# Kernel optimization log

Measured on AMD Instinct MI355X. Metric: run time of the kernel, lower is better.

## Reference

```python
import jax, jax.numpy as jnp
import numpy as np

N, E, F, FE, H, R = 100000, 3200000, 2, 7, 64, 500
BN_EPS = 1e-5
LEAKY_SLOPE = 0.01


def _bn(h, g, b):
    # BatchNorm1d in training mode: batch statistics over the node axis
    m = h.mean(0)
    v = h.var(0)
    return (h - m) * jax.lax.rsqrt(v + BN_EPS) * g + b


def _gine_conv(x, src, dst, edge_attr, eps, el_w, el_b, w1, b1, g, bt, w2, b2):
    # message: relu(x_j + Lin(edge_attr)); aggregate: scatter-add at dst
    msg = jax.nn.relu(x[src] + edge_attr @ el_w + el_b)          # [E, d]
    agg = jax.ops.segment_sum(msg, dst, num_segments=N)          # [N, d]
    h = (1.0 + eps) * x + agg
    # nn: Linear -> BN -> ReLU -> Linear -> ReLU
    h = jax.nn.relu(_bn(h @ w1 + b1, g, bt))
    return jax.nn.relu(h @ w2 + b2)


def setup_inputs() -> dict:
    key = jax.random.key(0)
    ks = jax.random.split(key, 16)
    r = lambda k, s, sc=0.1: jax.random.normal(k, s, dtype=jnp.float32) * sc
    return {
        "x": jax.random.normal(ks[0], (N, F), dtype=jnp.float32),
        "edge_attr": jax.random.normal(ks[1], (E, FE), dtype=jnp.float32),
        "edge_index": jax.random.randint(ks[2], (2, E), 0, N),
        "epoch": 1,
        "eps1": jnp.zeros((), jnp.float32),
        "el1_w": r(ks[3], (FE, F)), "el1_b": jnp.zeros((F,), jnp.float32),
        "n1_w1": r(ks[4], (F, H)), "n1_b1": jnp.zeros((H,), jnp.float32),
        "n1_g": jnp.ones((H,), jnp.float32), "n1_bt": jnp.zeros((H,), jnp.float32),
        "n1_w2": r(ks[5], (H, H)), "n1_b2": jnp.zeros((H,), jnp.float32),
        "eps2": jnp.zeros((), jnp.float32),
        "el2_w": r(ks[6], (FE, H)), "el2_b": jnp.zeros((H,), jnp.float32),
        "n2_w1": r(ks[7], (H, H)), "n2_b1": jnp.zeros((H,), jnp.float32),
        "n2_g": jnp.ones((H,), jnp.float32), "n2_bt": jnp.zeros((H,), jnp.float32),
        "n2_w2": r(ks[8], (H, H)), "n2_b2": jnp.zeros((H,), jnp.float32),
        "reg_w": r(ks[9], (H, R)), "reg_b": jnp.zeros((R,), jnp.float32),
        "end_w": r(ks[10], (R, 1)), "end_b": jnp.zeros((1,), jnp.float32),
    }


def reference(x, edge_attr, edge_index, epoch,
              eps1, el1_w, el1_b, n1_w1, n1_b1, n1_g, n1_bt, n1_w2, n1_b2,
              eps2, el2_w, el2_b, n2_w1, n2_b1, n2_g, n2_bt, n2_w2, n2_b2,
              reg_w, reg_b, end_w, end_b):
    src, dst = edge_index[0], edge_index[1]
    out = _gine_conv(x, src, dst, edge_attr, eps1, el1_w, el1_b,
                     n1_w1, n1_b1, n1_g, n1_bt, n1_w2, n1_b2)
    for _ in range(3 - 1):  # num_layers=3, shared conv2 weights
        out = _gine_conv(out, src, dst, edge_attr, eps2, el2_w, el2_b,
                         n2_w1, n2_b1, n2_g, n2_bt, n2_w2, n2_b2)
    # dropout p=0.0 -> identity; epoch only resets dropout, no effect here
    out = out @ reg_w + reg_b
    out = jnp.where(out >= 0, out, LEAKY_SLOPE * out)  # LeakyReLU
    out = out @ end_w + end_b                            # [N, 1]
    return out
```

## Files before the change

### kernel.cpp

```cpp
#include <hip/hip_runtime.h>
#include <hip/hip_fp16.h>

#define NN 100000
#define NE 3200000
#define NB 196
#define NCH 256
#define CH 12500

__device__ inline unsigned pkh(float a, float b) {
  __half2 h;
  h.x = __float2half(a);
  h.y = __float2half(b);
  unsigned u;
  __builtin_memcpy(&u, &h, 4);
  return u;
}
__device__ inline float2 uph(unsigned u) {
  __half2 h;
  __builtin_memcpy(&h, &u, 4);
  return __half22float2(h);
}
__device__ inline float h1f(unsigned short v) {
  __half h;
  __builtin_memcpy(&h, &v, 2);
  return __half2float(h);
}
__device__ inline unsigned short f1h(float f) {
  __half h = __float2half(f);
  unsigned short u;
  __builtin_memcpy(&u, &h, 2);
  return u;
}

__global__ __launch_bounds__(256) void count_kernel(const int* __restrict__ dst,
                                                    int* __restrict__ cnt) {
  int stride = gridDim.x * 256;
  for (int e = blockIdx.x * 256 + threadIdx.x; e < NE; e += stride)
    atomicAdd(&cnt[dst[e]], 1);
}

__global__ __launch_bounds__(1024) void scan_kernel(const int* __restrict__ cnt,
                                                    int* __restrict__ rowptr,
                                                    int* __restrict__ ofs) {
  __shared__ int bsum[1024];
  int tid = threadIdx.x;
  const int CHS = (NN + 1023) / 1024;
  int lo = tid * CHS, hi = lo + CHS < NN ? lo + CHS : NN;
  if (lo > NN) lo = NN;
  if (hi < lo) hi = lo;
  int s = 0;
  for (int i = lo; i < hi; i++) s += cnt[i];
  bsum[tid] = s;
  __syncthreads();
  for (int off = 1; off < 1024; off <<= 1) {
    int v = bsum[tid];
    int u = (tid >= off) ? bsum[tid - off] : 0;
    __syncthreads();
    bsum[tid] = v + u;
    __syncthreads();
  }
  int pre = (tid == 0) ? 0 : bsum[tid - 1];
  for (int i = lo; i < hi; i++) {
    int cv = cnt[i];
    rowptr[i] = pre;
    ofs[i] = pre;
    pre += cv;
  }
  if (tid == 1023) rowptr[NN] = pre;
}

__global__ __launch_bounds__(256) void binit_kernel(const int* __restrict__ rowptr,
                                                    int* __restrict__ binofs) {
  int t = threadIdx.x;
  if (t < NB) binofs[t] = rowptr[t * 512];
}

__global__ __launch_bounds__(256) void localsort_kernel(
    const int* __restrict__ src, const int* __restrict__ dst,
    const float* __restrict__ ea, int* __restrict__ binofs,
    uint4* __restrict__ stageR, int* __restrict__ stageS) {
  __shared__ int hist[NB];
  __shared__ int base[NB];
  int tid = threadIdx.x;
  int c0 = blockIdx.x * CH;
  int c1 = c0 + CH;
  if (tid < NB) hist[tid] = 0;
  __syncthreads();
  for (int e = c0 + tid; e < c1; e += 256)
    atomicAdd(&hist[dst[e] >> 9], 1);
  __syncthreads();
  if (tid < NB) {
    base[tid] = atomicAdd(&binofs[tid], hist[tid]);
    hist[tid] = 0;
  }
  __syncthreads();
  for (int e = c0 + tid; e < c1; e += 256) {
    int dn = dst[e];
    int sn = src[e];
    int b = dn >> 9;
    float av[7];
#pragma unroll
    for (int k = 0; k < 7; k++) av[k] = ea[e * 7 + k];
    int lp = atomicAdd(&hist[b], 1);
    int pos = base[b] + lp;
    uint4 r;
    r.x = pkh(av[0], av[1]);
    r.y = pkh(av[2], av[3]);
    r.z = pkh(av[4], av[5]);
    r.w = (unsigned)f1h(av[6]) | (((unsigned)dn & 511u) << 16);
    stageR[pos] = r;
    stageS[pos] = sn;
  }
}

__global__ __launch_bounds__(256) void binsort2_kernel(
    const int* __restrict__ rowptr, const uint4* __restrict__ stageR,
    const int* __restrict__ stageS, int* __restrict__ ofs,
    uint4* __restrict__ erec, int* __restrict__ esrc,
    const float* __restrict__ x, const float* __restrict__ elw,
    const float* __restrict__ elb, float* __restrict__ agg1) {
  float w0[7], w1r[7];
#pragma unroll
  for (int k = 0; k < 7; k++) { w0[k] = elw[k * 2]; w1r[k] = elw[k * 2 + 1]; }
  float b0 = elb[0], b1 = elb[1];
  int bin = blockIdx.x >> 1, half = blockIdx.x & 1;
  int nlo = bin * 512;
  int nhi = nlo + 512 < NN ? nlo + 512 : NN;
  int r0 = rowptr[nlo], r1 = rowptr[nhi];
  int mid = (r0 + r1) >> 1;
  int lo = half ? mid : r0;
  int hi = half ? r1 : mid;
  for (int i = lo + threadIdx.x; i < hi; i += 256) {
    uint4 u = stageR[i];
    int sn = stageS[i];
    int dn = nlo + (int)(u.w >> 16);
    int pos = atomicAdd(&ofs[dn], 1);
    erec[pos] = u;
    esrc[pos] = sn;
    float2 q0 = uph(u.x), q1 = uph(u.y), q2 = uph(u.z);
    float e6 = h1f((unsigned short)(u.w & 0xFFFFu));
    float m0 = b0, m1 = b1;
    m0 = fmaf(q0.x, w0[0], m0); m1 = fmaf(q0.x, w1r[0], m1);
    m0 = fmaf(q0.y, w0[1], m0); m1 = fmaf(q0.y, w1r[1], m1);
    m0 = fmaf(q1.x, w0[2], m0); m1 = fmaf(q1.x, w1r[2], m1);
    m0 = fmaf(q1.y, w0[3], m0); m1 = fmaf(q1.y, w1r[3], m1);
    m0 = fmaf(q2.x, w0[4], m0); m1 = fmaf(q2.x, w1r[4], m1);
    m0 = fmaf(q2.y, w0[5], m0); m1 = fmaf(q2.y, w1r[5], m1);
    m0 = fmaf(e6, w0[6], m0);   m1 = fmaf(e6, w1r[6], m1);
    m0 = fmaxf(m0 + x[sn * 2 + 0], 0.f);
    m1 = fmaxf(m1 + x[sn * 2 + 1], 0.f);
    unsafeAtomicAdd(&agg1[dn * 2 + 0], m0);
    unsafeAtomicAdd(&agg1[dn * 2 + 1], m1);
  }
}

__global__ __launch_bounds__(256) void scatter1_kernel(
    const int* __restrict__ dst, int* __restrict__ ofs, int* __restrict__ eid_s) {
  int stride = gridDim.x * 256;
  for (int e = blockIdx.x * 256 + threadIdx.x; e < NE; e += stride) {
    int pos = atomicAdd(&ofs[dst[e]], 1);
    eid_s[pos] = e;
  }
}

__global__ __launch_bounds__(256) void l1agg_kernel(
    const int* __restrict__ rowptr, const int* __restrict__ eid_s,
    const int* __restrict__ src, const float* __restrict__ ea,
    const float* __restrict__ x, const float* __restrict__ elw,
    const float* __restrict__ elb, float* __restrict__ agg) {
  float w0[7], w1r[7];
#pragma unroll
  for (int k = 0; k < 7; k++) { w0[k] = elw[k * 2]; w1r[k] = elw[k * 2 + 1]; }
  float b0 = elb[0], b1 = elb[1];
  int stride = gridDim.x * 256;
  for (int n = blockIdx.x * 256 + threadIdx.x; n < NN; n += stride) {
    int r0 = rowptr[n], r1 = rowptr[n + 1];
    float a0 = 0.f, a1 = 0.f;
    for (int i = r0; i < r1; i++) {
      int e = eid_s[i];
      int sn = src[e];
      float m0 = b0, m1 = b1;
#pragma unroll
      for (int k = 0; k < 7; k++) {
        float a = ea[e * 7 + k];
        m0 = fmaf(a, w0[k], m0);
        m1 = fmaf(a, w1r[k], m1);
      }
      m0 = fmaxf(m0 + x[sn * 2 + 0], 0.f);
      m1 = fmaxf(m1 + x[sn * 2 + 1], 0.f);
      a0 += m0; a1 += m1;
    }
    agg[n * 2 + 0] = a0;
    agg[n * 2 + 1] = a1;
  }
}

#define PROJH(m, u) do { \
  float2 q0 = uph((u).x), q1 = uph((u).y), q2 = uph((u).z), q3 = uph((u).w); \
  m = bel; \
  m = fmaf(q0.x, wel[0], m); m = fmaf(q0.y, wel[1], m); \
  m = fmaf(q1.x, wel[2], m); m = fmaf(q1.y, wel[3], m); \
  m = fmaf(q2.x, wel[4], m); m = fmaf(q2.y, wel[5], m); \
  m = fmaf(q3.x, wel[6], m); } while (0)

__global__ __launch_bounds__(256) void gine64h_kernel(
    const int* __restrict__ rowptr, const uint4* __restrict__ erec,
    const int* __restrict__ esrc, const float* __restrict__ xin,
    const unsigned short* __restrict__ xh, const float* __restrict__ elw,
    const float* __restrict__ elb, const float* __restrict__ w1,
    const float* __restrict__ b1, const float* __restrict__ eps_p,
    float* __restrict__ tbuf, float* __restrict__ stats) {
  __shared__ float wl[64 * 64];
  __shared__ float hb[4][64];
  __shared__ float red[256];
  int tid = threadIdx.x, lane = tid & 63, wv = tid >> 6;
  for (int i2 = tid; i2 < 64 * 64; i2 += 256) wl[i2] = w1[i2];
  float wel[7];
#pragma unroll
  for (int k = 0; k < 7; k++) wel[k] = elw[k * 64 + lane];
  float bel = elb[lane], b1c = b1[lane];
  float ep = 1.0f + *eps_p;
  float s = 0.f, ss = 0.f;
  __syncthreads();
  const unsigned short* xl = xh + lane;
  int nw = gridDim.x * 4;
  for (int n = blockIdx.x * 4 + wv; n < NN; n += nw) {
    int r0 = rowptr[n], r1 = rowptr[n + 1];
    float acc = 0.f;
    int i = r0;
    int rem = r1 - r0;
    if (rem >= 4) {
      uint4 u0 = erec[i], u1 = erec[i + 1], u2 = erec[i + 2], u3 = erec[i + 3];
      int s0 = esrc[i], s1 = esrc[i + 1], s2 = esrc[i + 2], s3 = esrc[i + 3];
      while (true) {
        float g0 = h1f(xl[s0 * 64]);
        float g1 = h1f(xl[s1 * 64]);
        float g2 = h1f(xl[s2 * 64]);
        float g3 = h1f(xl[s3 * 64]);
        i += 4; rem -= 4;
        bool more = rem >= 4;
        int ip = more ? i : r0;
        uint4 v0 = erec[ip], v1 = erec[ip + 1], v2 = erec[ip + 2], v3 = erec[ip + 3];
        int t0 = esrc[ip], t1 = esrc[ip + 1], t2 = esrc[ip + 2], t3 = esrc[ip + 3];
        float m0, m1, m2, m3;
        PROJH(m0, u0); PROJH(m1, u1); PROJH(m2, u2); PROJH(m3, u3);
        acc += fmaxf(m0 + g0, 0.f);
        acc += fmaxf(m1 + g1, 0.f);
        acc += fmaxf(m2 + g2, 0.f);
        acc += fmaxf(m3 + g3, 0.f);
        u0 = v0; u1 = v1; u2 = v2; u3 = v3;
        s0 = t0; s1 = t1; s2 = t2; s3 = t3;
        if (!more) break;
      }
    }
    for (; i < r1; i++) {
      uint4 u = erec[i];
      int sn = esrc[i];
      float m;
      PROJH(m, u);
      m += h1f(xl[sn * 64]);
      acc += fmaxf(m, 0.f);
    }
    float h = ep * xin[n * 64 + lane] + acc;
    hb[wv][lane] = h;
    float t = b1c;
#pragma unroll
    for (int k = 0; k < 64; k++) t = fmaf(hb[wv][k], wl[k * 64 + lane], t);
    tbuf[n * 64 + lane] = t;
    s += t;
    ss += t * t;
  }
  double* dsum = (double*)stats;
  red[tid] = s;
  __syncthreads();
  if (tid < 64) unsafeAtomicAdd(&dsum[tid], (double)(red[tid] + red[tid + 64] + red[tid + 128] + red[tid + 192]));
  __syncthreads();
  red[tid] = ss;
  __syncthreads();
  if (tid < 64) unsafeAtomicAdd(&dsum[64 + tid], (double)(red[tid] + red[tid + 64] + red[tid + 128] + red[tid + 192]));
}

__global__ __launch_bounds__(256) void gine64s_kernel(
    const int* __restrict__ rowptr, const int* __restrict__ eid_s,
    const int* __restrict__ src, const float* __restrict__ ea,
    const float* __restrict__ xin, const float* __restrict__ elw,
    const float* __restrict__ elb, const float* __restrict__ w1,
    const float* __restrict__ b1, const float* __restrict__ eps_p,
    float* __restrict__ tbuf, float* __restrict__ stats) {
  __shared__ float wl[64 * 64];
  __shared__ float hb[4][64];
  __shared__ float red[256];
  int tid = threadIdx.x, lane = tid & 63, wv = tid >> 6;
  for (int i = tid; i < 64 * 64; i += 256) wl[i] = w1[i];
  float wel[7];
#pragma unroll
  for (int k = 0; k < 7; k++) wel[k] = elw[k * 64 + lane];
  float bel = elb[lane], b1c = b1[lane];
  float ep = 1.0f + *eps_p;
  float s = 0.f, ss = 0.f;
  __syncthreads();
  int nw = gridDim.x * 4;
  for (int n = blockIdx.x * 4 + wv; n < NN; n += nw) {
    int r0 = rowptr[n], r1 = rowptr[n + 1];
    float acc = 0.f;
    for (int i = r0; i < r1; i++) {
      int e = eid_s[i];
      int sn = src[e];
      float m = bel;
#pragma unroll
      for (int k = 0; k < 7; k++) m = fmaf(ea[e * 7 + k], wel[k], m);
      m += xin[sn * 64 + lane];
      acc += fmaxf(m, 0.f);
    }
    float h = ep * xin[n * 64 + lane] + acc;
    hb[wv][lane] = h;
    float t = b1c;
#pragma unroll
    for (int k = 0; k < 64; k++) t = fmaf(hb[wv][k], wl[k * 64 + lane], t);
    tbuf[n * 64 + lane] = t;
    s += t;
    ss += t * t;
  }
  double* dsum = (double*)stats;
  red[tid] = s;
  __syncthreads();
  if (tid < 64) unsafeAtomicAdd(&dsum[tid], (double)(red[tid] + red[tid + 64] + red[tid + 128] + red[tid + 192]));
  __syncthreads();
  red[tid] = ss;
  __syncthreads();
  if (tid < 64) unsafeAtomicAdd(&dsum[64 + tid], (double)(red[tid] + red[tid + 64] + red[tid + 128] + red[tid + 192]));
}

__global__ __launch_bounds__(256) void edge1_kernel(
    const float* __restrict__ x, const float* __restrict__ ea,
    const int* __restrict__ src, const int* __restrict__ dst,
    const float* __restrict__ elw, const float* __restrict__ elb,
    float* __restrict__ agg) {
  float w0[7], w1[7];
#pragma unroll
  for (int k = 0; k < 7; k++) { w0[k] = elw[k * 2]; w1[k] = elw[k * 2 + 1]; }
  float b0 = elb[0], b1 = elb[1];
  int stride = gridDim.x * 256;
  for (int e = blockIdx.x * 256 + threadIdx.x; e < NE; e += stride) {
    int s = src[e], d = dst[e];
    float m0 = b0, m1 = b1;
#pragma unroll
    for (int k = 0; k < 7; k++) {
      float a = ea[e * 7 + k];
      m0 = fmaf(a, w0[k], m0);
      m1 = fmaf(a, w1[k], m1);
    }
    m0 = fmaxf(m0 + x[s * 2 + 0], 0.f);
    m1 = fmaxf(m1 + x[s * 2 + 1], 0.f);
    unsafeAtomicAdd(&agg[d * 2 + 0], m0);
    unsafeAtomicAdd(&agg[d * 2 + 1], m1);
  }
}

__global__ __launch_bounds__(256) void edge64_kernel(
    const float* __restrict__ xin, const float* __restrict__ ea,
    const int* __restrict__ src, const int* __restrict__ dst,
    const float* __restrict__ elw, const float* __restrict__ elb,
    float* __restrict__ agg) {
  int lane = threadIdx.x & 63;
  int wid = (blockIdx.x * 256 + threadIdx.x) >> 6;
  int nw = (gridDim.x * 256) >> 6;
  float w[7];
#pragma unroll
  for (int k = 0; k < 7; k++) w[k] = elw[k * 64 + lane];
  float b = elb[lane];
  for (int e = wid; e < NE; e += nw) {
    int eu = __builtin_amdgcn_readfirstlane(e);
    int s = src[eu];
    int d = dst[eu];
    float m = b;
#pragma unroll
    for (int k = 0; k < 7; k++) m = fmaf(ea[eu * 7 + k], w[k], m);
    m += xin[s * 64 + lane];
    m = fmaxf(m, 0.f);
    unsafeAtomicAdd(&agg[d * 64 + lane], m);
  }
}

__global__ __launch_bounds__(256) void nodeA64_kernel(
    const float* __restrict__ xin, float* __restrict__ tbuf,
    const float* __restrict__ w1, const float* __restrict__ b1,
    const float* __restrict__ eps_p, float* __restrict__ stats) {
  __shared__ float wl[64 * 64];
  __shared__ float hbuf[4][64];
  __shared__ float red[256];
  int tid = threadIdx.x;
  int c = tid & 63, nl = tid >> 6;
  for (int i = tid; i < 64 * 64; i += 256) wl[i] = w1[i];
  float ep = 1.0f + *eps_p;
  float bc = b1[c];
  float s = 0.f, ss = 0.f;
  __syncthreads();
  for (int n0 = blockIdx.x * 4; n0 < NN; n0 += gridDim.x * 4) {
    int n = n0 + nl;
    bool valid = n < NN;
    float h = 0.f;
    if (valid) h = ep * xin[n * 64 + c] + tbuf[n * 64 + c];
    hbuf[nl][c] = h;
    __syncthreads();
    if (valid) {
      float t = bc;
#pragma unroll
      for (int k = 0; k < 64; k++) t = fmaf(hbuf[nl][k], wl[k * 64 + c], t);
      tbuf[n * 64 + c] = t;
      s += t;
      ss += t * t;
    }
    __syncthreads();
  }
  double* dsum = (double*)stats;
  red[tid] = s;
  __syncthreads();
  if (tid < 64) unsafeAtomicAdd(&dsum[tid], (double)(red[tid] + red[tid + 64] + red[tid + 128] + red[tid + 192]));
  __syncthreads();
  red[tid] = ss;
  __syncthreads();
  if (tid < 64) unsafeAtomicAdd(&dsum[64 + tid], (double)(red[tid] + red[tid + 64] + red[tid + 128] + red[tid + 192]));
}

__global__ __launch_bounds__(256) void nodeA2_kernel(
    const float* __restrict__ x, const float* __restrict__ agg1,
    float* __restrict__ tbuf, const float* __restrict__ w1,
    const float* __restrict__ b1, const float* __restrict__ eps_p,
    float* __restrict__ stats) {
  __shared__ float red[256];
  int tid = threadIdx.x;
  int c = tid & 63, nl = tid >> 6;
  float wa = w1[c], wb = w1[64 + c], bc = b1[c];
  float ep = 1.0f + *eps_p;
  float s = 0.f, ss = 0.f;
  for (int n0 = blockIdx.x * 4; n0 < NN; n0 += gridDim.x * 4) {
    int n = n0 + nl;
    if (n < NN) {
      float h0 = ep * x[n * 2 + 0] + agg1[n * 2 + 0];
      float h1 = ep * x[n * 2 + 1] + agg1[n * 2 + 1];
      float t = fmaf(h1, wb, fmaf(h0, wa, bc));
      tbuf[n * 64 + c] = t;
      s += t;
      ss += t * t;
    }
  }
  double* dsum = (double*)stats;
  red[tid] = s;
  __syncthreads();
  if (tid < 64) unsafeAtomicAdd(&dsum[tid], (double)(red[tid] + red[tid + 64] + red[tid + 128] + red[tid + 192]));
  __syncthreads();
  red[tid] = ss;
  __syncthreads();
  if (tid < 64) unsafeAtomicAdd(&dsum[64 + tid], (double)(red[tid] + red[tid + 64] + red[tid + 128] + red[tid + 192]));
}

__global__ __launch_bounds__(256) void nodeB_kernel(
    const float* __restrict__ tin, float* __restrict__ outb,
    const float* __restrict__ w2, const float* __restrict__ b2,
    const float* __restrict__ stats, const float* __restrict__ g,
    const float* __restrict__ bt, unsigned short* __restrict__ xh) {
  __shared__ float wl[64 * 64];
  __shared__ float ubuf[4][64];
  __shared__ float scsh[128];
  int tid = threadIdx.x;
  int c = tid & 63, nl = tid >> 6;
  for (int i = tid; i < 64 * 64; i += 256) wl[i] = w2[i];
  if (tid < 64) {
    const double* ds = (const double*)stats;
    double m = ds[tid] / (double)NN;
    double v = ds[64 + tid] / (double)NN - m * m;
    float sc = g[tid] * (float)(1.0 / sqrt(v + 1e-5));
    scsh[tid] = sc;
    scsh[64 + tid] = bt[tid] - (float)m * sc;
  }
  float bc = b2[c];
  __syncthreads();
  float scale = scsh[c], shift = scsh[64 + c];
  for (int n0 = blockIdx.x * 4; n0 < NN; n0 += gridDim.x * 4) {
    int n = n0 + nl;
    bool valid = n < NN;
    float u = 0.f;
    if (valid) {
      float t = tin[n * 64 + c];
      u = fmaxf(fmaf(t, scale, shift), 0.f);
    }
    ubuf[nl][c] = u;
    __syncthreads();
    if (valid) {
      float o = bc;
#pragma unroll
      for (int k = 0; k < 64; k++) o = fmaf(ubuf[nl][k], wl[k * 64 + c], o);
      o = fmaxf(o, 0.f);
      outb[n * 64 + c] = o;
      if (xh) xh[n * 64 + c] = f1h(o);
    }
    __syncthreads();
  }
}

__global__ __launch_bounds__(256) void final_kernel(
    const float* __restrict__ xin, const float* __restrict__ regw,
    const float* __restrict__ regb, const float* __restrict__ endw,
    const float* __restrict__ endb, float* __restrict__ out) {
  __shared__ float wl[64 * 128];
  __shared__ float eb[256];
  int tid = threadIdx.x;
  int node = blockIdx.x * 256 + tid;
  bool valid = node < NN;
  float xr[64];
  if (valid) {
    const float4* xp = (const float4*)(xin + node * 64);
#pragma unroll
    for (int k4 = 0; k4 < 16; k4++) {
      float4 v = xp[k4];
      xr[k4 * 4 + 0] = v.x; xr[k4 * 4 + 1] = v.y;
      xr[k4 * 4 + 2] = v.z; xr[k4 * 4 + 3] = v.w;
    }
  }
  float y = 0.f;
  for (int ch = 0; ch < 4; ch++) {
    int j0 = ch * 125;
    __syncthreads();
    for (int idx = tid; idx < 64 * 125; idx += 256) {
      int k = idx / 125;
      int jl = idx - k * 125;
      wl[k * 128 + jl] = regw[k * 500 + j0 + jl];
    }
    if (tid < 125) { eb[tid] = regb[j0 + tid]; eb[128 + tid] = endw[j0 + tid]; }
    __syncthreads();
    if (valid) {
      int jl = 0;
      for (; jl + 4 <= 125; jl += 4) {
        float t0 = eb[jl], t1 = eb[jl + 1], t2 = eb[jl + 2], t3 = eb[jl + 3];
#pragma unroll
        for (int k = 0; k < 64; k++) {
          float4 w4 = *(const float4*)&wl[k * 128 + jl];
          float xv = xr[k];
          t0 = fmaf(xv, w4.x, t0);
          t1 = fmaf(xv, w4.y, t1);
          t2 = fmaf(xv, w4.z, t2);
          t3 = fmaf(xv, w4.w, t3);
        }
        t0 = t0 >= 0.f ? t0 : 0.01f * t0;
        t1 = t1 >= 0.f ? t1 : 0.01f * t1;
        t2 = t2 >= 0.f ? t2 : 0.01f * t2;
        t3 = t3 >= 0.f ? t3 : 0.01f * t3;
        y += t0 * eb[128 + jl] + t1 * eb[128 + jl + 1] + t2 * eb[128 + jl + 2] + t3 * eb[128 + jl + 3];
      }
      {
        float t = eb[124];
#pragma unroll
        for (int k = 0; k < 64; k++) t = fmaf(xr[k], wl[k * 128 + 124], t);
        t = t >= 0.f ? t : 0.01f * t;
        y += t * eb[128 + 124];
      }
    }
  }
  if (valid) out[node] = y + endb[0];
}

extern "C" void kernel_launch(void* const* d_in, const int* in_sizes, int n_in,
                              void* d_out, int out_size, void* d_ws, size_t ws_size,
                              hipStream_t stream) {
  const float* x    = (const float*)d_in[0];
  const float* ea   = (const float*)d_in[1];
  const int*   ei   = (const int*)d_in[2];
  const float* eps1 = (const float*)d_in[4];
  const float* el1w = (const float*)d_in[5];
  const float* el1b = (const float*)d_in[6];
  const float* n1w1 = (const float*)d_in[7];
  const float* n1b1 = (const float*)d_in[8];
  const float* n1g  = (const float*)d_in[9];
  const float* n1bt = (const float*)d_in[10];
  const float* n1w2 = (const float*)d_in[11];
  const float* n1b2 = (const float*)d_in[12];
  const float* eps2 = (const float*)d_in[13];
  const float* el2w = (const float*)d_in[14];
  const float* el2b = (const float*)d_in[15];
  const float* n2w1 = (const float*)d_in[16];
  const float* n2b1 = (const float*)d_in[17];
  const float* n2g  = (const float*)d_in[18];
  const float* n2bt = (const float*)d_in[19];
  const float* n2w2 = (const float*)d_in[20];
  const float* n2b2 = (const float*)d_in[21];
  const float* regw = (const float*)d_in[22];
  const float* regb = (const float*)d_in[23];
  const float* endw = (const float*)d_in[24];
  const float* endb = (const float*)d_in[25];
  const int* srcp = ei;
  const int* dstp = ei + NE;

  const size_t o_stats  = 0;
  const size_t o_agg1   = 768;
  const size_t o_cnt    = 200768;
  const size_t o_rowptr = 300768;
  const size_t o_binofs = 400772;
  const size_t o_buf0   = 401032;
  const size_t o_buf1   = 6801032;
  const size_t o_xh     = 13201032;
  const size_t o_erec   = 16401032;
  const size_t o_esrc   = 29201032;
  const size_t needA2 = (o_esrc + (size_t)NE) * 4;
  const size_t needA1 = (o_erec + (size_t)NE) * 4;
  const size_t needB  = (2 * 6600000 + 384) * 4;

  float* wsf = (float*)d_ws;

  if (ws_size >= needA1) {
    const bool packed = ws_size >= needA2;
    float* stats0 = wsf + o_stats;
    float* stats1 = wsf + o_stats + 256;
    float* stats2 = wsf + o_stats + 512;
    float* agg1  = wsf + o_agg1;
    int* cnt     = (int*)(wsf + o_cnt);
    int* rowptr  = (int*)(wsf + o_rowptr);
    int* binofs  = (int*)(wsf + o_binofs);
    float* buf0  = wsf + o_buf0;
    float* buf1  = wsf + o_buf1;
    unsigned short* xh = (unsigned short*)(wsf + o_xh);
    uint4* erec  = (uint4*)(wsf + o_erec);
    int* esrc    = (int*)(wsf + o_esrc);
    uint4* stageR = (uint4*)(wsf + o_buf0);
    int* stageS   = (int*)(wsf + o_xh);

    hipMemsetAsync(wsf, 0, (768 + 200000 + NN) * sizeof(float), stream);

    count_kernel<<<4096, 256, 0, stream>>>(dstp, cnt);
    scan_kernel<<<1, 1024, 0, stream>>>(cnt, rowptr, cnt);
    if (packed) {
      binit_kernel<<<1, 256, 0, stream>>>(rowptr, binofs);
      localsort_kernel<<<NCH, 256, 0, stream>>>(srcp, dstp, ea, binofs,
                                                stageR, stageS);
      binsort2_kernel<<<NB * 2, 256, 0, stream>>>(rowptr, stageR, stageS, cnt,
                                                  erec, esrc, x, el1w, el1b, agg1);
    } else {
      scatter1_kernel<<<4096, 256, 0, stream>>>(dstp, cnt, (int*)(wsf + o_erec));
      l1agg_kernel<<<391, 256, 0, stream>>>(rowptr, (const int*)(wsf + o_erec),
                                            srcp, ea, x, el1w, el1b, agg1);
    }

    nodeA2_kernel<<<2048, 256, 0, stream>>>(x, agg1, buf1, n1w1, n1b1, eps1, stats0);
    nodeB_kernel<<<2048, 256, 0, stream>>>(buf1, buf1, n1w2, n1b2, stats0,
                                           n1g, n1bt, packed ? xh : nullptr);

    if (packed) {
      gine64h_kernel<<<4096, 256, 0, stream>>>(rowptr, erec, esrc, buf1, xh,
                                               el2w, el2b, n2w1, n2b1, eps2,
                                               buf0, stats1);
      nodeB_kernel<<<2048, 256, 0, stream>>>(buf0, buf0, n2w2, n2b2, stats1,
                                             n2g, n2bt, xh);
      gine64h_kernel<<<4096, 256, 0, stream>>>(rowptr, erec, esrc, buf0, xh,
                                               el2w, el2b, n2w1, n2b1, eps2,
                                               buf1, stats2);
      nodeB_kernel<<<2048, 256, 0, stream>>>(buf1, buf1, n2w2, n2b2, stats2,
                                             n2g, n2bt, nullptr);
      final_kernel<<<(NN + 255) / 256, 256, 0, stream>>>(buf1, regw, regb, endw,
                                                         endb, (float*)d_out);
    } else {
      float* cur = buf1;
      float* wrk = buf0;
      float* sl[2] = {stats1, stats2};
      for (int l = 0; l < 2; l++) {
        gine64s_kernel<<<4096, 256, 0, stream>>>(rowptr, (const int*)(wsf + o_erec),
                                                 srcp, ea, cur, el2w, el2b, n2w1,
                                                 n2b1, eps2, wrk, sl[l]);
        nodeB_kernel<<<2048, 256, 0, stream>>>(wrk, wrk, n2w2, n2b2, sl[l],
                                               n2g, n2bt, nullptr);
        float* tmp = cur; cur = wrk; wrk = tmp;
      }
      final_kernel<<<(NN + 255) / 256, 256, 0, stream>>>(cur, regw, regb, endw,
                                                         endb, (float*)d_out);
    }
    return;
  }

  if (ws_size < needB) return;
  const size_t BUF = 6600000;
  float* buf0 = (float*)d_ws;
  float* buf1 = buf0 + BUF;
  float* stats = buf1 + BUF;

  float* t1 = buf1;
  float* agg1 = buf1 + NN * 64;
  hipMemsetAsync(agg1, 0, NN * 2 * sizeof(float), stream);
  hipMemsetAsync(stats, 0, 128 * sizeof(double), stream);
  edge1_kernel<<<2048, 256, 0, stream>>>(x, ea, srcp, dstp, el1w, el1b, agg1);
  nodeA2_kernel<<<2048, 256, 0, stream>>>(x, agg1, t1, n1w1, n1b1, eps1, stats);
  nodeB_kernel<<<2048, 256, 0, stream>>>(t1, buf1, n1w2, n1b2, stats, n1g, n1bt,
                                         nullptr);

  float* cur = buf1;
  float* wrk = buf0;
  for (int l = 0; l < 2; l++) {
    hipMemsetAsync(wrk, 0, NN * 64 * sizeof(float), stream);
    hipMemsetAsync(stats, 0, 128 * sizeof(double), stream);
    edge64_kernel<<<2048, 256, 0, stream>>>(cur, ea, srcp, dstp, el2w, el2b, wrk);
    nodeA64_kernel<<<2048, 256, 0, stream>>>(cur, wrk, n2w1, n2b1, eps2, stats);
    nodeB_kernel<<<2048, 256, 0, stream>>>(wrk, wrk, n2w2, n2b2, stats, n2g, n2bt,
                                           nullptr);
    float* tmp = cur; cur = wrk; wrk = tmp;
  }

  final_kernel<<<(NN + 255) / 256, 256, 0, stream>>>(cur, regw, regb, endw, endb,
                                                     (float*)d_out);
}
```

Baseline: 1.531 ms.

## Replace full CSR sort with 128-node bin partition and shared-memory aggregation

Drops the per-node CSR build (count, scan, second-level sort into erec/esrc). Edges are now partitioned into 128-node bins with a deterministic per-block histogram, scan and scatter. The layer kernels process each bin in one block and accumulate messages into a 128x64 shared-memory tile using LDS atomics instead of per-node register sums. This removes a full global sort pass and the global atomics, but adds LDS atomic contention and 32KB+ of shared memory per block, which lowers occupancy. Only 782 blocks are launched, and load balance now depends on bin sizes.

Result: slower. 3.286 ms (+114.6%).

```diff
diff --git a/kernel.cpp b/kernel.cpp
--- a/kernel.cpp
+++ b/kernel.cpp
@@ -3,9 +3,9 @@
 
 #define NN 100000
 #define NE 3200000
-#define NB 196
-#define NCH 256
-#define CH 12500
+#define NBIN 782
+#define NBLK 256
+#define CHE 12500
 
 __device__ inline unsigned pkh(float a, float b) {
   __half2 h;
@@ -30,6 +30,211 @@
   unsigned short u;
   __builtin_memcpy(&u, &h, 2);
   return u;
+}
+
+__global__ __launch_bounds__(256) void histk_kernel(const int* __restrict__ dst,
+                                                    int* __restrict__ blkhist) {
+  __shared__ int hist[NBIN];
+  int tid = threadIdx.x;
+  for (int i = tid; i < NBIN; i += 256) hist[i] = 0;
+  __syncthreads();
+  int c0 = blockIdx.x * CHE, c1 = c0 + CHE;
+  for (int e = c0 + tid; e < c1; e += 256) atomicAdd(&hist[dst[e] >> 7], 1);
+  __syncthreads();
+  for (int i = tid; i < NBIN; i += 256)
+    blkhist[blockIdx.x * NBIN + i] = hist[i];
+}
+
+__global__ __launch_bounds__(1024) void scank_kernel(int* __restrict__ blkhist,
+                                                     int* __restrict__ binstart) {
+  __shared__ int tot[1024];
+  int b = threadIdx.x;
+  int running = 0;
+  if (b < NBIN) {
+    for (int blk = 0; blk < NBLK; blk++) {
+      int v = blkhist[blk * NBIN + b];
+      blkhist[blk * NBIN + b] = running;
+      running += v;
+    }
+  }
+  tot[b] = (b < NBIN) ? running : 0;
+  __syncthreads();
+  for (int off = 1; off < 1024; off <<= 1) {
+    int v = tot[b];
+    int u = (b >= off) ? tot[b - off] : 0;
+    __syncthreads();
+    tot[b] = v + u;
+    __syncthreads();
+  }
+  int start = (b == 0) ? 0 : tot[b - 1];
+  if (b < NBIN) {
+    binstart[b] = start;
+    for (int blk = 0; blk < NBLK; blk++) blkhist[blk * NBIN + b] += start;
+  }
+  if (b == 0) binstart[NBIN] = tot[1023];
+}
+
+__global__ __launch_bounds__(256) void scatk_kernel(
+    const int* __restrict__ src, const int* __restrict__ dst,
+    const float* __restrict__ ea, const int* __restrict__ blkhist,
+    uint4* __restrict__ stageR, int* __restrict__ stageS) {
+  __shared__ int ofs[NBIN];
+  int tid = threadIdx.x;
+  for (int i = tid; i < NBIN; i += 256)
+    ofs[i] = blkhist[blockIdx.x * NBIN + i];
+  __syncthreads();
+  int c0 = blockIdx.x * CHE, c1 = c0 + CHE;
+  for (int e = c0 + tid; e < c1; e += 256) {
+    int dn = dst[e];
+    int sn = src[e];
+    float av[7];
+#pragma unroll
+    for (int k = 0; k < 7; k++) av[k] = ea[e * 7 + k];
+    int pos = atomicAdd(&ofs[dn >> 7], 1);
+    uint4 r;
+    r.x = pkh(av[0], av[1]);
+    r.y = pkh(av[2], av[3]);
+    r.z = pkh(av[4], av[5]);
+    r.w = (unsigned)f1h(av[6]) | (((unsigned)dn & 127u) << 16);
+    stageR[pos] = r;
+    stageS[pos] = sn;
+  }
+}
+
+__global__ __launch_bounds__(256) void gine2b_kernel(
+    const int* __restrict__ binstart, const uint4* __restrict__ stageR,
+    const int* __restrict__ stageS, const float* __restrict__ x,
+    const float* __restrict__ elw, const float* __restrict__ elb,
+    float* __restrict__ agg1) {
+  __shared__ float acc[128][2];
+  int tid = threadIdx.x;
+  float w0[7], w1r[7];
+#pragma unroll
+  for (int k = 0; k < 7; k++) { w0[k] = elw[k * 2]; w1r[k] = elw[k * 2 + 1]; }
+  float b0 = elb[0], b1 = elb[1];
+  if (tid < 128) { acc[tid][0] = 0.f; acc[tid][1] = 0.f; }
+  __syncthreads();
+  int r0 = binstart[blockIdx.x], r1 = binstart[blockIdx.x + 1];
+  for (int i = r0 + tid; i < r1; i += 256) {
+    uint4 u = stageR[i];
+    int sn = stageS[i];
+    int ln = (int)((u.w >> 16) & 127u);
+    float2 q0 = uph(u.x), q1 = uph(u.y), q2 = uph(u.z);
+    float e6 = h1f((unsigned short)(u.w & 0xFFFFu));
+    float m0 = b0, m1 = b1;
+    m0 = fmaf(q0.x, w0[0], m0); m1 = fmaf(q0.x, w1r[0], m1);
+    m0 = fmaf(q0.y, w0[1], m0); m1 = fmaf(q0.y, w1r[1], m1);
+    m0 = fmaf(q1.x, w0[2], m0); m1 = fmaf(q1.x, w1r[2], m1);
+    m0 = fmaf(q1.y, w0[3], m0); m1 = fmaf(q1.y, w1r[3], m1);
+    m0 = fmaf(q2.x, w0[4], m0); m1 = fmaf(q2.x, w1r[4], m1);
+    m0 = fmaf(q2.y, w0[5], m0); m1 = fmaf(q2.y, w1r[5], m1);
+    m0 = fmaf(e6, w0[6], m0);   m1 = fmaf(e6, w1r[6], m1);
+    m0 = fmaxf(m0 + x[sn * 2 + 0], 0.f);
+    m1 = fmaxf(m1 + x[sn * 2 + 1], 0.f);
+    atomicAdd(&acc[ln][0], m0);
+    atomicAdd(&acc[ln][1], m1);
+  }
+  __syncthreads();
+  int n = (blockIdx.x << 7) + tid;
+  if (tid < 128 && n < NN) {
+    agg1[n * 2 + 0] = acc[tid][0];
+    agg1[n * 2 + 1] = acc[tid][1];
+  }
+}
+
+#define PROJH(m, u) do { \
+  float2 q0 = uph((u).x), q1 = uph((u).y), q2 = uph((u).z), q3 = uph((u).w); \
+  m = bel; \
+  m = fmaf(q0.x, wel[0], m); m = fmaf(q0.y, wel[1], m); \
+  m = fmaf(q1.x, wel[2], m); m = fmaf(q1.y, wel[3], m); \
+  m = fmaf(q2.x, wel[4], m); m = fmaf(q2.y, wel[5], m); \
+  m = fmaf(q3.x, wel[6], m); } while (0)
+
+__global__ __launch_bounds__(256) void gine64b_kernel(
+    const int* __restrict__ binstart, const uint4* __restrict__ stageR,
+    const int* __restrict__ stageS, const float* __restrict__ xin,
+    const unsigned short* __restrict__ xh, const float* __restrict__ elw,
+    const float* __restrict__ elb, const float* __restrict__ w1,
+    const float* __restrict__ b1, const float* __restrict__ eps_p,
+    float* __restrict__ tbuf, float* __restrict__ stats) {
+  __shared__ float wl[64 * 64];
+  __shared__ float acc[128][64];
+  __shared__ float hb[4][64];
+  __shared__ float red[256];
+  int tid = threadIdx.x, lane = tid & 63, wv = tid >> 6;
+  for (int i2 = tid; i2 < 64 * 64; i2 += 256) wl[i2] = w1[i2];
+  float wel[7];
+#pragma unroll
+  for (int k = 0; k < 7; k++) wel[k] = elw[k * 64 + lane];
+  float bel = elb[lane], b1c = b1[lane];
+  float ep = 1.0f + *eps_p;
+  for (int i2 = tid; i2 < 128 * 64; i2 += 256) ((float*)acc)[i2] = 0.f;
+  __syncthreads();
+  int r0 = binstart[blockIdx.x], r1 = binstart[blockIdx.x + 1];
+  int len = r1 - r0;
+  int per = (len + 3) >> 2;
+  int lo = r0 + wv * per;
+  int hi = lo + per < r1 ? lo + per : r1;
+  if (lo > r1) lo = r1;
+  const unsigned short* xl = xh + lane;
+  int i = lo;
+  if (hi - lo >= 4) {
+    uint4 u0 = stageR[i], u1 = stageR[i + 1], u2 = stageR[i + 2], u3 = stageR[i + 3];
+    int s0 = stageS[i], s1 = stageS[i + 1], s2 = stageS[i + 2], s3 = stageS[i + 3];
+    while (true) {
+      float g0 = h1f(xl[s0 * 64]);
+      float g1 = h1f(xl[s1 * 64]);
+      float g2 = h1f(xl[s2 * 64]);
+      float g3 = h1f(xl[s3 * 64]);
+      i += 4;
+      bool more = (hi - i) >= 4;
+      int ip = more ? i : lo;
+      uint4 v0 = stageR[ip], v1 = stageR[ip + 1], v2 = stageR[ip + 2], v3 = stageR[ip + 3];
+      int t0 = stageS[ip], t1 = stageS[ip + 1], t2 = stageS[ip + 2], t3 = stageS[ip + 3];
+      float m0, m1, m2, m3;
+      PROJH(m0, u0); PROJH(m1, u1); PROJH(m2, u2); PROJH(m3, u3);
+      int d0 = (int)((u0.w >> 16) & 127u), d1 = (int)((u1.w >> 16) & 127u);
+      int d2 = (int)((u2.w >> 16) & 127u), d3 = (int)((u3.w >> 16) & 127u);
+      atomicAdd(&acc[d0][lane], fmaxf(m0 + g0, 0.f));
+      atomicAdd(&acc[d1][lane], fmaxf(m1 + g1, 0.f));
+      atomicAdd(&acc[d2][lane], fmaxf(m2 + g2, 0.f));
+      atomicAdd(&acc[d3][lane], fmaxf(m3 + g3, 0.f));
+      u0 = v0; u1 = v1; u2 = v2; u3 = v3;
+      s0 = t0; s1 = t1; s2 = t2; s3 = t3;
+      if (!more) break;
+    }
+  }
+  for (; i < hi; i++) {
+    uint4 u = stageR[i];
+    int sn = stageS[i];
+    float m;
+    PROJH(m, u);
+    int d = (int)((u.w >> 16) & 127u);
+    atomicAdd(&acc[d][lane], fmaxf(m + h1f(xl[sn * 64]), 0.f));
+  }
+  __syncthreads();
+  int n0 = blockIdx.x << 7;
+  float s = 0.f, ss = 0.f;
+  for (int j = wv; j < 128; j += 4) {
+    int n = n0 + j;
+    if (n >= NN) break;
+    float h = ep * xin[n * 64 + lane] + acc[j][lane];
+    hb[wv][lane] = h;
+    float t = b1c;
+#pragma unroll
+    for (int k = 0; k < 64; k++) t = fmaf(hb[wv][k], wl[k * 64 + lane], t);
+    tbuf[n * 64 + lane] = t;
+    s += t;
+    ss += t * t;
+  }
+  double* dsum = (double*)stats;
+  red[tid] = s;
+  __syncthreads();
+  if (tid < 64) unsafeAtomicAdd(&dsum[tid], (double)(red[tid] + red[tid + 64] + red[tid + 128] + red[tid + 192]));
+  __syncthreads();
+  red[tid] = ss;
+  __syncthreads();
+  if (tid < 64) unsafeAtomicAdd(&dsum[64 + tid], (double)(red[tid] + red[tid + 64] + red[tid + 128] + red[tid + 192]));
 }
 
 __global__ __launch_bounds__(256) void count_kernel(const int* __restrict__ dst,
@@ -69,91 +274,6 @@
   if (tid == 1023) rowptr[NN] = pre;
 }
 
-__global__ __launch_bounds__(256) void binit_kernel(const int* __restrict__ rowptr,
-                                                    int* __restrict__ binofs) {
-  int t = threadIdx.x;
-  if (t < NB) binofs[t] = rowptr[t * 512];
-}
-
-__global__ __launch_bounds__(256) void localsort_kernel(
-    const int* __restrict__ src, const int* __restrict__ dst,
-    const float* __restrict__ ea, int* __restrict__ binofs,
-    uint4* __restrict__ stageR, int* __restrict__ stageS) {
-  __shared__ int hist[NB];
-  __shared__ int base[NB];
-  int tid = threadIdx.x;
-  int c0 = blockIdx.x * CH;
-  int c1 = c0 + CH;
-  if (tid < NB) hist[tid] = 0;
-  __syncthreads();
-  for (int e = c0 + tid; e < c1; e += 256)
-    atomicAdd(&hist[dst[e] >> 9], 1);
-  __syncthreads();
-  if (tid < NB) {
-    base[tid] = atomicAdd(&binofs[tid], hist[tid]);
-    hist[tid] = 0;
-  }
-  __syncthreads();
-  for (int e = c0 + tid; e < c1; e += 256) {
-    int dn = dst[e];
-    int sn = src[e];
-    int b = dn >> 9;
-    float av[7];
-#pragma unroll
-    for (int k = 0; k < 7; k++) av[k] = ea[e * 7 + k];
-    int lp = atomicAdd(&hist[b], 1);
-    int pos = base[b] + lp;
-    uint4 r;
-    r.x = pkh(av[0], av[1]);
-    r.y = pkh(av[2], av[3]);
-    r.z = pkh(av[4], av[5]);
-    r.w = (unsigned)f1h(av[6]) | (((unsigned)dn & 511u) << 16);
-    stageR[pos] = r;
-    stageS[pos] = sn;
-  }
-}
-
-__global__ __launch_bounds__(256) void binsort2_kernel(
-    const int* __restrict__ rowptr, const uint4* __restrict__ stageR,
-    const int* __restrict__ stageS, int* __restrict__ ofs,
-    uint4* __restrict__ erec, int* __restrict__ esrc,
-    const float* __restrict__ x, const float* __restrict__ elw,
-    const float* __restrict__ elb, float* __restrict__ agg1) {
-  float w0[7], w1r[7];
-#pragma unroll
-  for (int k = 0; k < 7; k++) { w0[k] = elw[k * 2]; w1r[k] = elw[k * 2 + 1]; }
-  float b0 = elb[0], b1 = elb[1];
-  int bin = blockIdx.x >> 1, half = blockIdx.x & 1;
-  int nlo = bin * 512;
-  int nhi = nlo + 512 < NN ? nlo + 512 : NN;
-  int r0 = rowptr[nlo], r1 = rowptr[nhi];
-  int mid = (r0 + r1) >> 1;
-  int lo = half ? mid : r0;
-  int hi = half ? r1 : mid;
-  for (int i = lo + threadIdx.x; i < hi; i += 256) {
-    uint4 u = stageR[i];
-    int sn = stageS[i];
-    int dn = nlo + (int)(u.w >> 16);
-    int pos = atomicAdd(&ofs[dn], 1);
-    erec[pos] = u;
-    esrc[pos] = sn;
-    float2 q0 = uph(u.x), q1 = uph(u.y), q2 = uph(u.z);
-    float e6 = h1f((unsigned short)(u.w & 0xFFFFu));
-    float m0 = b0, m1 = b1;
-    m0 = fmaf(q0.x, w0[0], m0); m1 = fmaf(q0.x, w1r[0], m1);
-    m0 = fmaf(q0.y, w0[1], m0); m1 = fmaf(q0.y, w1r[1], m1);
-    m0 = fmaf(q1.x, w0[2], m0); m1 = fmaf(q1.x, w1r[2], m1);
-    m0 = fmaf(q1.y, w0[3], m0); m1 = fmaf(q1.y, w1r[3], m1);
-    m0 = fmaf(q2.x, w0[4], m0); m1 = fmaf(q2.x, w1r[4], m1);
-    m0 = fmaf(q2.y, w0[5], m0); m1 = fmaf(q2.y, w1r[5], m1);
-    m0 = fmaf(e6, w0[6], m0);   m1 = fmaf(e6, w1r[6], m1);
-    m0 = fmaxf(m0 + x[sn * 2 + 0], 0.f);
-    m1 = fmaxf(m1 + x[sn * 2 + 1], 0.f);
-    unsafeAtomicAdd(&agg1[dn * 2 + 0], m0);
-    unsafeAtomicAdd(&agg1[dn * 2 + 1], m1);
-  }
-}
-
 __global__ __launch_bounds__(256) void scatter1_kernel(
     const int* __restrict__ dst, int* __restrict__ ofs, int* __restrict__ eid_s) {
   int stride = gridDim.x * 256;
@@ -193,91 +313,6 @@
     agg[n * 2 + 0] = a0;
     agg[n * 2 + 1] = a1;
   }
-}
-
-#define PROJH(m, u) do { \
-  float2 q0 = uph((u).x), q1 = uph((u).y), q2 = uph((u).z), q3 = uph((u).w); \
-  m = bel; \
-  m = fmaf(q0.x, wel[0], m); m = fmaf(q0.y, wel[1], m); \
-  m = fmaf(q1.x, wel[2], m); m = fmaf(q1.y, wel[3], m); \
-  m = fmaf(q2.x, wel[4], m); m = fmaf(q2.y, wel[5], m); \
-  m = fmaf(q3.x, wel[6], m); } while (0)
-
-__global__ __launch_bounds__(256) void gine64h_kernel(
-    const int* __restrict__ rowptr, const uint4* __restrict__ erec,
-    const int* __restrict__ esrc, const float* __restrict__ xin,
-    const unsigned short* __restrict__ xh, const float* __restrict__ elw,
-    const float* __restrict__ elb, const float* __restrict__ w1,
-    const float* __restrict__ b1, const float* __restrict__ eps_p,
-    float* __restrict__ tbuf, float* __restrict__ stats) {
-  __shared__ float wl[64 * 64];
-  __shared__ float hb[4][64];
-  __shared__ float red[256];
-  int tid = threadIdx.x, lane = tid & 63, wv = tid >> 6;
-  for (int i2 = tid; i2 < 64 * 64; i2 += 256) wl[i2] = w1[i2];
-  float wel[7];
-#pragma unroll
-  for (int k = 0; k < 7; k++) wel[k] = elw[k * 64 + lane];
-  float bel = elb[lane], b1c = b1[lane];
-  float ep = 1.0f + *eps_p;
-  float s = 0.f, ss = 0.f;
-  __syncthreads();
-  const unsigned short* xl = xh + lane;
-  int nw = gridDim.x * 4;
-  for (int n = blockIdx.x * 4 + wv; n < NN; n += nw) {
-    int r0 = rowptr[n], r1 = rowptr[n + 1];
-    float acc = 0.f;
-    int i = r0;
-    int rem = r1 - r0;
-    if (rem >= 4) {
-      uint4 u0 = erec[i], u1 = erec[i + 1], u2 = erec[i + 2], u3 = erec[i + 3];
-      int s0 = esrc[i], s1 = esrc[i + 1], s2 = esrc[i + 2], s3 = esrc[i + 3];
-      while (true) {
-        float g0 = h1f(xl[s0 * 64]);
-        float g1 = h1f(xl[s1 * 64]);
-        float g2 = h1f(xl[s2 * 64]);
-        float g3 = h1f(xl[s3 * 64]);
-        i += 4; rem -= 4;
-        bool more = rem >= 4;
-        int ip = more ? i : r0;
-        uint4 v0 = erec[ip], v1 = erec[ip + 1], v2 = erec[ip + 2], v3 = erec[ip + 3];
-        int t0 = esrc[ip], t1 = esrc[ip + 1], t2 = esrc[ip + 2], t3 = esrc[ip + 3];
-        float m0, m1, m2, m3;
-        PROJH(m0, u0); PROJH(m1, u1); PROJH(m2, u2); PROJH(m3, u3);
-        acc += fmaxf(m0 + g0, 0.f);
-        acc += fmaxf(m1 + g1, 0.f);
-        acc += fmaxf(m2 + g2, 0.f);
-        acc += fmaxf(m3 + g3, 0.f);
-        u0 = v0; u1 = v1; u2 = v2; u3 = v3;
-        s0 = t0; s1 = t1; s2 = t2; s3 = t3;
-        if (!more) break;
-      }
-    }
-    for (; i < r1; i++) {
-      uint4 u = erec[i];
-      int sn = esrc[i];
-      float m;
-      PROJH(m, u);
-      m += h1f(xl[sn * 64]);
-      acc += fmaxf(m, 0.f);
-    }
-    float h = ep * xin[n * 64 + lane] + acc;
-    hb[wv][lane] = h;
-    float t = b1c;
-#pragma unroll
-    for (int k = 0; k < 64; k++) t = fmaf(hb[wv][k], wl[k * 64 + lane], t);
-    tbuf[n * 64 + lane] = t;
-    s += t;
-    ss += t * t;
-  }
-  double* dsum = (double*)stats;
-  red[tid] = s;
-  __syncthreads();
-  if (tid < 64) unsafeAtomicAdd(&dsum[tid], (double)(red[tid] + red[tid + 64] + red[tid + 128] + red[tid + 192]));
-  __syncthreads();
-  red[tid] = ss;
-  __syncthreads();
-  if (tid < 64) unsafeAtomicAdd(&dsum[64 + tid], (double)(red[tid] + red[tid + 64] + red[tid + 128] + red[tid + 192]));
 }
 
 __global__ __launch_bounds__(256) void gine64s_kernel(
@@ -591,87 +626,96 @@
   const int* srcp = ei;
   const int* dstp = ei + NE;
 
-  const size_t o_stats  = 0;
-  const size_t o_agg1   = 768;
-  const size_t o_cnt    = 200768;
-  const size_t o_rowptr = 300768;
-  const size_t o_binofs = 400772;
-  const size_t o_buf0   = 401032;
-  const size_t o_buf1   = 6801032;
-  const size_t o_xh     = 13201032;
-  const size_t o_erec   = 16401032;
-  const size_t o_esrc   = 29201032;
-  const size_t needA2 = (o_esrc + (size_t)NE) * 4;
-  const size_t needA1 = (o_erec + (size_t)NE) * 4;
+  const size_t o_stats    = 0;
+  const size_t o_binstart = 768;
+  const size_t o_share    = 1552;
+  const size_t o_buf0     = 201744;
+  const size_t o_buf1     = 6601744;
+  const size_t o_xh       = 13001744;
+  const size_t o_aggslim  = 16201744;
+  const size_t o_stageR   = 16201744;
+  const size_t o_stageS   = 29001744;
+  const size_t needA2 = (o_stageS + (size_t)NE) * 4;
+  const size_t needA1 = (o_aggslim + (size_t)NN * 2) * 4;
   const size_t needB  = (2 * 6600000 + 384) * 4;
 
   float* wsf = (float*)d_ws;
 
-  if (ws_size >= needA1) {
-    const bool packed = ws_size >= needA2;
+  if (ws_size >= needA2) {
     float* stats0 = wsf + o_stats;
     float* stats1 = wsf + o_stats + 256;
     float* stats2 = wsf + o_stats + 512;
-    float* agg1  = wsf + o_agg1;
-    int* cnt     = (int*)(wsf + o_cnt);
-    int* rowptr  = (int*)(wsf + o_rowptr);
-    int* binofs  = (int*)(wsf + o_binofs);
-    float* buf0  = wsf + o_buf0;
-    float* buf1  = wsf + o_buf1;
+    int* binstart = (int*)(wsf + o_binstart);
+    int* blkhist  = (int*)(wsf + o_share);
+    float* agg1   = wsf + o_share;
+    float* buf0   = wsf + o_buf0;
+    float* buf1   = wsf + o_buf1;
     unsigned short* xh = (unsigned short*)(wsf + o_xh);
-    uint4* erec  = (uint4*)(wsf + o_erec);
-    int* esrc    = (int*)(wsf + o_esrc);
-    uint4* stageR = (uint4*)(wsf + o_buf0);
-    int* stageS   = (int*)(wsf + o_xh);
-
-    hipMemsetAsync(wsf, 0, (768 + 200000 + NN) * sizeof(float), stream);
-
+    uint4* stageR = (uint4*)(wsf + o_stageR);
+    int* stageS   = (int*)(wsf + o_stageS);
+
+    hipMemsetAsync(wsf, 0, 768 * sizeof(float), stream);
+
+    histk_kernel<<<NBLK, 256, 0, stream>>>(dstp, blkhist);
+    scank_kernel<<<1, 1024, 0, stream>>>(blkhist, binstart);
+    scatk_kernel<<<NBLK, 256, 0, stream>>>(srcp, dstp, ea, blkhist,
+                                           stageR, stageS);
+
+    gine2b_kernel<<<NBIN, 256, 0, stream>>>(binstart, stageR, stageS, x,
+                                            el1w, el1b, agg1);
+    nodeA2_kernel<<<2048, 256, 0, stream>>>(x, agg1, buf1, n1w1, n1b1, eps1, stats0);
+    nodeB_kernel<<<2048, 256, 0, stream>>>(buf1, buf1, n1w2, n1b2, stats0,
+                                           n1g, n1bt, xh);
+
+    gine64b_kernel<<<NBIN, 256, 0, stream>>>(binstart, stageR, stageS, buf1, xh,
+                                             el2w, el2b, n2w1, n2b1, eps2,
+                                             buf0, stats1);
+    nodeB_kernel<<<2048, 256, 0, stream>>>(buf0, buf0, n2w2, n2b2, stats1,
+                                           n2g, n2bt, xh);
+    gine64b_kernel<<<NBIN, 256, 0, stream>>>(binstart, stageR, stageS, buf0, xh,
+                                             el2w, el2b, n2w1, n2b1, eps2,
+                                             buf1, stats2);
+    nodeB_kernel<<<2048, 256, 0, stream>>>(buf1, buf1, n2w2, n2b2, stats2,
+                                           n2g, n2bt, nullptr);
+    final_kernel<<<(NN + 255) / 256, 256, 0, stream>>>(buf1, regw, regb, endw,
+                                                       endb, (float*)d_out);
+    return;
+  }
+
+  if (ws_size >= needA1) {
+    float* stats0 = wsf + o_stats;
+    float* stats1 = wsf + o_stats + 256;
+    float* stats2 = wsf + o_stats + 512;
+    int* cnt    = (int*)(wsf + o_share);
+    int* rowptr = (int*)(wsf + o_share) + NN;
+    float* buf0 = wsf + o_buf0;
+    float* buf1 = wsf + o_buf1;
+    int* eid    = (int*)(wsf + o_xh);
+    float* agg1 = wsf + o_aggslim;
+
+    hipMemsetAsync(wsf, 0, 768 * sizeof(float), stream);
+    hipMemsetAsync(cnt, 0, NN * sizeof(int), stream);
     count_kernel<<<4096, 256, 0, stream>>>(dstp, cnt);
     scan_kernel<<<1, 1024, 0, stream>>>(cnt, rowptr, cnt);
-    if (packed) {
-      binit_kernel<<<1, 256, 0, stream>>>(rowptr, binofs);
-      localsort_kernel<<<NCH, 256, 0, stream>>>(srcp, dstp, ea, binofs,
-                                                stageR, stageS);
-      binsort2_kernel<<<NB * 2, 256, 0, stream>>>(rowptr, stageR, stageS, cnt,
-                                                  erec, esrc, x, el1w, el1b, agg1);
-    } else {
-      scatter1_kernel<<<4096, 256, 0, stream>>>(dstp, cnt, (int*)(wsf + o_erec));
-      l1agg_kernel<<<391, 256, 0, stream>>>(rowptr, (const int*)(wsf + o_erec),
-                                            srcp, ea, x, el1w, el1b, agg1);
-    }
-
+    scatter1_kernel<<<4096, 256, 0, stream>>>(dstp, cnt, eid);
+    l1agg_kernel<<<391, 256, 0, stream>>>(rowptr, eid, srcp, ea, x, el1w, el1b,
+                                          agg1);
     nodeA2_kernel<<<2048, 256, 0, stream>>>(x, agg1, buf1, n1w1, n1b1, eps1, stats0);
     nodeB_kernel<<<2048, 256, 0, stream>>>(buf1, buf1, n1w2, n1b2, stats0,
-                                           n1g, n1bt, packed ? xh : nullptr);
-
-    if (packed) {
-      gine64h_kernel<<<4096, 256, 0, stream>>>(rowptr, erec, esrc, buf1, xh,
+                                           n1g, n1bt, nullptr);
+    float* cur = buf1;
+    float* wrk = buf0;
+    float* sl[2] = {stats1, stats2};
+    for (int l = 0; l < 2; l++) {
+      gine64s_kernel<<<4096, 256, 0, stream>>>(rowptr, eid, srcp, ea, cur,
                                                el2w, el2b, n2w1, n2b1, eps2,
-                                               buf0, stats1);
-      nodeB_kernel<<<2048, 256, 0, stream>>>(buf0, buf0, n2w2, n2b2, stats1,
-                                             n2g, n2bt, xh);
-      gine64h_kernel<<<4096, 256, 0, stream>>>(rowptr, erec, esrc, buf0, xh,
-                                               el2w, el2b, n2w1, n2b1, eps2,
-                                               buf1, stats2);
-      nodeB_kernel<<<2048, 256, 0, stream>>>(buf1, buf1, n2w2, n2b2, stats2,
+                                               wrk, sl[l]);
+      nodeB_kernel<<<2048, 256, 0, stream>>>(wrk, wrk, n2w2, n2b2, sl[l],
                                              n2g, n2bt, nullptr);
-      final_kernel<<<(NN + 255) / 256, 256, 0, stream>>>(buf1, regw, regb, endw,
-                                                         endb, (float*)d_out);
-    } else {
-      float* cur = buf1;
-      float* wrk = buf0;
-      float* sl[2] = {stats1, stats2};
-      for (int l = 0; l < 2; l++) {
-        gine64s_kernel<<<4096, 256, 0, stream>>>(rowptr, (const int*)(wsf + o_erec),
-                                                 srcp, ea, cur, el2w, el2b, n2w1,
-                                                 n2b1, eps2, wrk, sl[l]);
-        nodeB_kernel<<<2048, 256, 0, stream>>>(wrk, wrk, n2w2, n2b2, sl[l],
-                                               n2g, n2bt, nullptr);
-        float* tmp = cur; cur = wrk; wrk = tmp;
-      }
-      final_kernel<<<(NN + 255) / 256, 256, 0, stream>>>(cur, regw, regb, endw,
-                                                         endb, (float*)d_out);
-    }
+      float* tmp = cur; cur = wrk; wrk = tmp;
+    }
+    final_kernel<<<(NN + 255) / 256, 256, 0, stream>>>(cur, regw, regb, endw,
+                                                       endb, (float*)d_out);
     return;
   }
 
```
